# Kernel optimization log

Hardware: AMD Instinct MI355X
Metric: run time of the kernel (lower is better)

The kernel has to match this reference:

```python
import jax, jax.numpy as jnp
import numpy as np
import math

B, L, C = 1, 4096, 1024
H = 16
D = C // H  # head_dim = 64


def setup_inputs() -> dict:
    key = jax.random.key(0)
    ks = jax.random.split(key, 5)
    s = 1.0 / math.sqrt(C)
    return {
        "x": jax.random.normal(ks[0], (B, L, C), dtype=jnp.float32),
        "Wq": jax.random.normal(ks[1], (C, C), dtype=jnp.float32) * s,
        "Wk": jax.random.normal(ks[2], (C, C), dtype=jnp.float32) * s,
        "Wv": jax.random.normal(ks[3], (C, C), dtype=jnp.float32) * s,
        "Wo": jax.random.normal(ks[4], (C, C), dtype=jnp.float32) * s,
    }


def reference(x, Wq, Wk, Wv, Wo):
    # Projections (bias=False). Wq etc. are applied as x @ W (equivalent
    # parameterization to torch Linear's x @ W.T with transposed storage).
    q = (x @ Wq).reshape(B, L, H, D).transpose(0, 2, 1, 3)  # (B,H,L,D)
    k = (x @ Wk).reshape(B, L, H, D).transpose(0, 2, 1, 3)
    v = (x @ Wv).reshape(B, L, H, D).transpose(0, 2, 1, 3)

    scale = 1.0 / math.sqrt(D)
    scores = jnp.einsum("bhqd,bhkd->bhqk", q, k) * scale  # (B,H,L,L)
    causal = jnp.tril(jnp.ones((L, L), dtype=bool))
    scores = jnp.where(causal[None, None, :, :], scores, -jnp.inf)
    probs = jax.nn.softmax(scores, axis=-1)  # dropout p=0 -> identity

    out = jnp.einsum("bhqk,bhkd->bhqd", probs, v)  # (B,H,L,D)
    out = out.transpose(0, 2, 1, 3).reshape(B, L, C)
    return out @ Wo  # resid dropout p=0 -> identity
```

## Files before the change

### kernel.cpp

```cpp
#include <hip/hip_runtime.h>

#define L_SEQ 4096
#define C_DIM 1024
#define H_NUM 16
#define D_HEAD 64
#define LDQK 2048

typedef __bf16 bf16x8 __attribute__((ext_vector_type(8)));
typedef __bf16 bf16x4 __attribute__((ext_vector_type(4)));
typedef float f32x4 __attribute__((ext_vector_type(4)));
typedef float f32x16 __attribute__((ext_vector_type(16)));
typedef unsigned int u32;
typedef u32 u32x4 __attribute__((ext_vector_type(4)));

#define AS1 __attribute__((address_space(1)))
#define AS3 __attribute__((address_space(3)))

#define SC_LOG2E 0.1803368801111204f

__device__ inline __bf16 f2bf(float f) {
  unsigned u = __builtin_bit_cast(unsigned, f);
  u = (u + 0x7fffu + ((u >> 16) & 1u)) >> 16;
  unsigned short s = (unsigned short)u;
  return __builtin_bit_cast(__bf16, s);
}

__device__ inline void gload_lds16(const __bf16* g, __bf16* l) {
  __builtin_amdgcn_global_load_lds((const AS1 void*)g, (AS3 void*)l, 16, 0, 0);
}

__global__ __launch_bounds__(256) void prep(const float* __restrict__ x,
                                            const float* __restrict__ W0,
                                            const float* __restrict__ W1,
                                            const float* __restrict__ W2,
                                            const float* __restrict__ W3,
                                            __bf16* __restrict__ xb,
                                            __bf16* __restrict__ Wt) {
  __shared__ float t[32][33];
  int id = blockIdx.x;
  if (id < 4096) {
    int i = (id * 256 + threadIdx.x) * 4;
    float4 v = *(const float4*)(x + i);
    bf16x4 o = {f2bf(v.x), f2bf(v.y), f2bf(v.z), f2bf(v.w)};
    *(bf16x4*)(xb + i) = o;
    return;
  }
  id -= 4096;
  const int z = id >> 10;
  const int rem = id & 1023;
  const float* W = (z == 0) ? W0 : (z == 1) ? W1 : (z == 2) ? W2 : W3;
  __bf16* dst = Wt + (size_t)z * 1048576;
  const int tx = threadIdx.x & 31, ty = threadIdx.x >> 5;
  const int c0 = (rem & 31) * 32, r0 = (rem >> 5) * 32;
#pragma unroll
  for (int k = 0; k < 4; ++k)
    t[ty + k * 8][tx] = W[(size_t)(r0 + ty + k * 8) * C_DIM + c0 + tx];
  __syncthreads();
#pragma unroll
  for (int k = 0; k < 4; ++k)
    dst[(size_t)(c0 + ty + k * 8) * C_DIM + r0 + tx] = f2bf(t[tx][ty + k * 8]);
}

__global__ __launch_bounds__(256) void gemm_qkv(const __bf16* __restrict__ xb,
                                                const __bf16* __restrict__ WqkT,
                                                const __bf16* __restrict__ WvT,
                                                __bf16* __restrict__ QKb,
                                                __bf16* __restrict__ Vtb) {
  __shared__ __bf16 As[128 * 32];
  __shared__ __bf16 Bs[128 * 32];
  int g = blockIdx.x;
  const __bf16 *A, *Bt;
  __bf16* C;
  int N;
  size_t arow0, brow0;
  float esc;
  if (g < 512) {
    A = xb; Bt = WqkT; C = QKb; N = 2048;
    arow0 = (size_t)(g & 31) * 128;
    brow0 = (size_t)(g >> 5) * 128;
    esc = ((int)brow0 < 1024) ? SC_LOG2E : 1.0f;
  } else {
    g -= 512;
    A = WvT; Bt = xb; C = Vtb; N = 4096;
    arow0 = (size_t)(g & 7) * 128;
    brow0 = (size_t)(g >> 3) * 128;
    esc = 1.0f;
  }
  const int K = 1024;

  const int tid = threadIdx.x;
  const int lane = tid & 63;
  const int wave = tid >> 6;
  const int wm = wave >> 1, wn = wave & 1;
  const int c16 = lane & 15, g4 = lane >> 4;
  const int srow = lane >> 2, scol = (lane & 3) * 8;

  f32x4 acc[4][4] = {};

  for (int kt = 0; kt < K; kt += 32) {
#pragma unroll
    for (int i = 0; i < 2; ++i) {
      const int row = i * 64 + wave * 16 + srow;
      gload_lds16(A + (arow0 + row) * K + kt + scol, As + (i * 64 + wave * 16) * 32);
      gload_lds16(Bt + (brow0 + row) * K + kt + scol, Bs + (i * 64 + wave * 16) * 32);
    }
    __syncthreads();
    bf16x8 af[4], bfr[4];
#pragma unroll
    for (int mi = 0; mi < 4; ++mi)
      af[mi] = *(const bf16x8*)(As + (wm * 64 + mi * 16 + c16) * 32 + g4 * 8);
#pragma unroll
    for (int ni = 0; ni < 4; ++ni)
      bfr[ni] = *(const bf16x8*)(Bs + (wn * 64 + ni * 16 + c16) * 32 + g4 * 8);
#pragma unroll
    for (int mi = 0; mi < 4; ++mi)
#pragma unroll
      for (int ni = 0; ni < 4; ++ni)
        acc[mi][ni] = __builtin_amdgcn_mfma_f32_16x16x32_bf16(af[mi], bfr[ni], acc[mi][ni], 0, 0, 0);
    __syncthreads();
  }

#pragma unroll
  for (int mi = 0; mi < 4; ++mi)
#pragma unroll
    for (int ni = 0; ni < 4; ++ni)
#pragma unroll
      for (int i = 0; i < 4; ++i) {
        size_t row = arow0 + wm * 64 + mi * 16 + g4 * 4 + i;
        size_t col = brow0 + wn * 64 + ni * 16 + c16;
        C[row * N + col] = f2bf(acc[mi][ni][i] * esc);
      }
}

template <bool OUT_BF16>
__global__ __launch_bounds__(256) void gemm_bt(const __bf16* __restrict__ A,
                                               const __bf16* __restrict__ Bt,
                                               void* __restrict__ Cp,
                                               int M, int N, int K,
                                               float cscale, int scale_ncols) {
  __shared__ __bf16 As[128 * 32];
  __shared__ __bf16 Bs[128 * 32];
  const int tid = threadIdx.x;
  const int lane = tid & 63;
  const int wave = tid >> 6;
  const int wm = wave >> 1, wn = wave & 1;
  const int c16 = lane & 15, g4 = lane >> 4;
  const int srow = lane >> 2, scol = (lane & 3) * 8;

  f32x4 acc[4][4] = {};

  const size_t arow0 = (size_t)blockIdx.x * 128;
  const size_t brow0 = (size_t)blockIdx.y * 128;

  for (int kt = 0; kt < K; kt += 32) {
#pragma unroll
    for (int i = 0; i < 2; ++i) {
      const int row = i * 64 + wave * 16 + srow;
      gload_lds16(A + (arow0 + row) * K + kt + scol, As + (i * 64 + wave * 16) * 32);
      gload_lds16(Bt + (brow0 + row) * K + kt + scol, Bs + (i * 64 + wave * 16) * 32);
    }
    __syncthreads();
    bf16x8 af[4], bfr[4];
#pragma unroll
    for (int mi = 0; mi < 4; ++mi)
      af[mi] = *(const bf16x8*)(As + (wm * 64 + mi * 16 + c16) * 32 + g4 * 8);
#pragma unroll
    for (int ni = 0; ni < 4; ++ni)
      bfr[ni] = *(const bf16x8*)(Bs + (wn * 64 + ni * 16 + c16) * 32 + g4 * 8);
#pragma unroll
    for (int mi = 0; mi < 4; ++mi)
#pragma unroll
      for (int ni = 0; ni < 4; ++ni)
        acc[mi][ni] = __builtin_amdgcn_mfma_f32_16x16x32_bf16(af[mi], bfr[ni], acc[mi][ni], 0, 0, 0);
    __syncthreads();
  }

  const float esc = ((int)brow0 < scale_ncols) ? cscale : 1.0f;
#pragma unroll
  for (int mi = 0; mi < 4; ++mi)
#pragma unroll
    for (int ni = 0; ni < 4; ++ni)
#pragma unroll
      for (int i = 0; i < 4; ++i) {
        size_t row = arow0 + wm * 64 + mi * 16 + g4 * 4 + i;
        size_t col = brow0 + wn * 64 + ni * 16 + c16;
        if (OUT_BF16)
          ((__bf16*)Cp)[row * N + col] = f2bf(acc[mi][ni][i] * esc);
        else
          ((float*)Cp)[row * N + col] = acc[mi][ni][i];
      }
}

__global__ __launch_bounds__(256, 1) void attn_fwd(const __bf16* __restrict__ Q,
                                                   const __bf16* __restrict__ Kg,
                                                   const __bf16* __restrict__ Vt,
                                                   __bf16* __restrict__ O) {
  const int bid = blockIdx.x;
  const int h = bid & 15;
  const int p = bid >> 4;
  const int qtA = 31 - p, qtB = p;
  const int ntA = 2 * qtA + 2;
  const int NT = 66;

  __shared__ __bf16 Ks[3][64 * 64];
  __shared__ __bf16 Vs[3][64 * 64];
  __shared__ __bf16 PoS[4][2048];

  const int tid = threadIdx.x;
  const int lane = tid & 63;
  const int wave = tid >> 6;
  const int l31 = lane & 31;
  const int hl = lane >> 5;
  const int rl = lane >> 3;
  const int cs = (lane & 7) ^ rl;

  auto stage = [&](int idx, int b) {
    const int kv = (idx < ntA) ? idx : idx - ntA;
#pragma unroll
    for (int i = 0; i < 2; ++i) {
      const int r = (i * 4 + wave) * 8 + rl;
      gload_lds16(Kg + (size_t)(kv * 64 + r) * LDQK + h * D_HEAD + cs * 8,
                  &Ks[b][(i * 4 + wave) * 512]);
      gload_lds16(Vt + (size_t)(h * D_HEAD + r) * L_SEQ + kv * 64 + cs * 8,
                  &Vs[b][(i * 4 + wave) * 512]);
    }
  };

  int qbase = qtA * 128 + wave * 32;
  bf16x8 qf[4], qfB[4];
  {
    const __bf16* qp = Q + (size_t)(qbase + l31) * LDQK + h * D_HEAD + hl * 8;
#pragma unroll
    for (int s = 0; s < 4; ++s) qf[s] = *(const bf16x8*)(qp + s * 16);
    const __bf16* qp2 = Q + (size_t)(qtB * 128 + wave * 32 + l31) * LDQK + h * D_HEAD + hl * 8;
#pragma unroll
    for (int s = 0; s < 4; ++s) qfB[s] = *(const bf16x8*)(qp2 + s * 16);
  }

  stage(0, 0);
  stage(1, 1);

  int kvmax_w = 2 * qtA + (wave >> 1);
  int q = qbase + l31;

  f32x16 acc0 = {}, acc1 = {};
  float m = -1e30f, lsum = 0.f;
  int bc = 0;

  auto epilogue = [&]() {
    const float rinv = 1.0f / lsum;
    char* const Po = (char*)&PoS[wave][0];
#pragma unroll
    for (int dt = 0; dt < 2; ++dt) {
#pragma unroll
      for (int i = 0; i < 8; ++i) {
        const int r = 2 * i;
        const int d = dt * 32 + (r & 3) + 8 * (r >> 2) + 4 * hl;
        float lo = (dt ? acc1[r] : acc0[r]) * rinv;
        float hi = (dt ? acc1[r + 1] : acc0[r + 1]) * rinv;
        u32 wv;
        asm("v_cvt_pk_bf16_f32 %0, %1, %2" : "=v"(wv) : "v"(lo), "v"(hi));
        *(u32*)(Po + l31 * 128 + (((d >> 3) ^ (l31 & 7)) << 4) + (d & 7) * 2) = wv;
      }
    }
    asm volatile("s_waitcnt lgkmcnt(0)" ::: "memory");
    __builtin_amdgcn_sched_barrier(0);
#pragma unroll
    for (int j = 0; j < 4; ++j) {
      const int qr = lane >> 1;
      const int c = (lane & 1) * 4 + j;
      bf16x8 ov = *(const bf16x8*)(Po + qr * 128 + ((c ^ (qr & 7)) << 4));
      *(bf16x8*)(O + (size_t)(qbase + qr) * C_DIM + h * D_HEAD + c * 8) = ov;
    }
  };

  for (int idx = 0; idx < NT; ++idx) {
    __builtin_amdgcn_sched_barrier(0);
    __builtin_amdgcn_s_barrier();
    __builtin_amdgcn_sched_barrier(0);

    if (idx + 2 < NT) {
      int bs = bc + 2; if (bs >= 3) bs -= 3;
      stage(idx + 2, bs);
      asm volatile("s_waitcnt vmcnt(8)" ::: "memory");
    } else if (idx + 2 == NT) {
      asm volatile("s_waitcnt vmcnt(4)" ::: "memory");
    } else {
      asm volatile("s_waitcnt vmcnt(0)" ::: "memory");
    }
    __builtin_amdgcn_sched_barrier(0);

    const int kvl = (idx < ntA) ? idx : idx - ntA;

    if (kvl <= kvmax_w) {
      char* const KsB = (char*)&Ks[bc][0];
      char* const VsB = (char*)&Vs[bc][0];

      f32x16 st0 = {}, st1 = {};
      __builtin_amdgcn_s_setprio(1);
#pragma unroll
      for (int s = 0; s < 4; ++s) {
        const int ch = s * 2 + hl;
        bf16x8 a0 = *(const bf16x8*)(KsB + l31 * 128 + ((ch ^ (l31 & 7)) << 4));
        bf16x8 a1 = *(const bf16x8*)(KsB + (32 + l31) * 128 + ((ch ^ (l31 & 7)) << 4));
        st0 = __builtin_amdgcn_mfma_f32_32x32x16_bf16(a0, qf[s], st0, 0, 0, 0);
        st1 = __builtin_amdgcn_mfma_f32_32x32x16_bf16(a1, qf[s], st1, 0, 0, 0);
      }
      __builtin_amdgcn_s_setprio(0);

      if (kvl == kvmax_w) {
#pragma unroll
        for (int r = 0; r < 16; ++r) {
          const int kr = (r & 3) + 8 * (r >> 2) + 4 * hl;
          const int k0 = kvl * 64 + kr;
          st0[r] = (k0 <= q) ? st0[r] : -1e30f;
          st1[r] = (k0 + 32 <= q) ? st1[r] : -1e30f;
        }
      }

      float t[16];
#pragma unroll
      for (int r = 0; r < 16; ++r) t[r] = fmaxf(st0[r], st1[r]);
#pragma unroll
      for (int w = 8; w > 0; w >>= 1)
#pragma unroll
        for (int r = 0; r < w; ++r) t[r] = fmaxf(t[r], t[r + w]);
      float mx = fmaxf(t[0], __shfl_xor(t[0], 32, 64));
      const float mnew = fmaxf(m, mx);
      const float corr = exp2f(m - mnew);
      m = mnew;

#pragma unroll
      for (int r = 0; r < 16; ++r) {
        st0[r] = exp2f(st0[r] - m);
        st1[r] = exp2f(st1[r] - m);
      }
      float sm[16];
#pragma unroll
      for (int r = 0; r < 16; ++r) sm[r] = st0[r] + st1[r];
#pragma unroll
      for (int w = 8; w > 0; w >>= 1)
#pragma unroll
        for (int r = 0; r < w; ++r) sm[r] = sm[r] + sm[r + w];
      float sl = sm[0] + __shfl_xor(sm[0], 32, 64);
      lsum = lsum * corr + sl;
      acc0 *= corr;
      acc1 *= corr;

      u32 w0[8], w1[8];
#pragma unroll
      for (int i = 0; i < 8; ++i) {
        asm("v_cvt_pk_bf16_f32 %0, %1, %2" : "=v"(w0[i]) : "v"(st0[2 * i]), "v"(st0[2 * i + 1]));
        asm("v_cvt_pk_bf16_f32 %0, %1, %2" : "=v"(w1[i]) : "v"(st1[2 * i]), "v"(st1[2 * i + 1]));
      }
      u32 e0a = (u32)__shfl_xor((int)(hl ? w0[0] : w0[2]), 32, 64);
      u32 e0b = (u32)__shfl_xor((int)(hl ? w0[1] : w0[3]), 32, 64);
      u32 e0c = (u32)__shfl_xor((int)(hl ? w0[4] : w0[6]), 32, 64);
      u32 e0d = (u32)__shfl_xor((int)(hl ? w0[5] : w0[7]), 32, 64);
      u32 e1a = (u32)__shfl_xor((int)(hl ? w1[0] : w1[2]), 32, 64);
      u32 e1b = (u32)__shfl_xor((int)(hl ? w1[1] : w1[3]), 32, 64);
      u32 e1c = (u32)__shfl_xor((int)(hl ? w1[4] : w1[6]), 32, 64);
      u32 e1d = (u32)__shfl_xor((int)(hl ? w1[5] : w1[7]), 32, 64);
      u32x4 f0 = hl ? (u32x4){e0a, e0b, w0[2], w0[3]} : (u32x4){w0[0], w0[1], e0a, e0b};
      u32x4 f1 = hl ? (u32x4){e0c, e0d, w0[6], w0[7]} : (u32x4){w0[4], w0[5], e0c, e0d};
      u32x4 f2 = hl ? (u32x4){e1a, e1b, w1[2], w1[3]} : (u32x4){w1[0], w1[1], e1a, e1b};
      u32x4 f3 = hl ? (u32x4){e1c, e1d, w1[6], w1[7]} : (u32x4){w1[4], w1[5], e1c, e1d};
      bf16x8 pb0 = __builtin_bit_cast(bf16x8, f0);
      bf16x8 pb1 = __builtin_bit_cast(bf16x8, f1);
      bf16x8 pb2 = __builtin_bit_cast(bf16x8, f2);
      bf16x8 pb3 = __builtin_bit_cast(bf16x8, f3);

      __builtin_amdgcn_s_setprio(1);
#pragma unroll
      for (int s = 0; s < 4; ++s) {
        const bf16x8 pb = (s == 0) ? pb0 : (s == 1) ? pb1 : (s == 2) ? pb2 : pb3;
        const int ch = s * 2 + hl;
        bf16x8 va0 = *(const bf16x8*)(VsB + l31 * 128 + ((ch ^ (l31 & 7)) << 4));
        bf16x8 va1 = *(const bf16x8*)(VsB + (32 + l31) * 128 + ((ch ^ (l31 & 7)) << 4));
        acc0 = __builtin_amdgcn_mfma_f32_32x32x16_bf16(va0, pb, acc0, 0, 0, 0);
        acc1 = __builtin_amdgcn_mfma_f32_32x32x16_bf16(va1, pb, acc1, 0, 0, 0);
      }
      __builtin_amdgcn_s_setprio(0);
    }

    if (idx == ntA - 1) {
      epilogue();
      qbase = qtB * 128 + wave * 32;
      q = qbase + l31;
      kvmax_w = 2 * qtB + (wave >> 1);
#pragma unroll
      for (int s = 0; s < 4; ++s) qf[s] = qfB[s];
      acc0 = (f32x16){};
      acc1 = (f32x16){};
      m = -1e30f;
      lsum = 0.f;
    }

    bc = (bc + 1 == 3) ? 0 : bc + 1;
  }

  epilogue();
}

extern "C" void kernel_launch(void* const* d_in, const int* in_sizes, int n_in,
                              void* d_out, int out_size, void* d_ws, size_t ws_size,
                              hipStream_t stream) {
  const float* x = (const float*)d_in[0];
  const float* Wq = (const float*)d_in[1];
  const float* Wk = (const float*)d_in[2];
  const float* Wv = (const float*)d_in[3];
  const float* Wo = (const float*)d_in[4];
  float* out = (float*)d_out;

  char* ws = (char*)d_ws;
  __bf16* xb    = (__bf16*)(ws);
  __bf16* WqkvT = (__bf16*)(ws + (8u << 20));
  __bf16* QKb   = (__bf16*)(ws + (16u << 20));
  __bf16* Vtb   = (__bf16*)(ws + (32u << 20));
  __bf16* WvT   = WqkvT + (size_t)2 * 1048576;
  __bf16* WoT   = WqkvT + (size_t)3 * 1048576;
  __bf16* Ab    = xb;

  prep<<<8192, 256, 0, stream>>>(x, Wq, Wk, Wv, Wo, xb, WqkvT);

  gemm_qkv<<<768, 256, 0, stream>>>(xb, WqkvT, WvT, QKb, Vtb);

  attn_fwd<<<256, 256, 0, stream>>>(QKb, QKb + 1024, Vtb, Ab);

  gemm_bt<false><<<dim3(32, 8), 256, 0, stream>>>(
      Ab, WoT, out, L_SEQ, C_DIM, C_DIM, 1.0f, 0);
}
```

Before: 275.3 us.

## Split paired-tile attention blocks into one q-tile per block with 2 blocks/CU

Each attention block used to process two complementary query tiles (long and short) in sequence so that work per block stayed balanced. Now each block handles a single 128-row query tile, the grid doubles to 512 blocks, and launch bounds allow 2 blocks per CU so the hardware can overlap them. The K/V prefetch depth also drops from two tiles ahead to one. Block ordering puts the long tiles first, leaving the short tiles to fill in at the end. The risks are tighter register pressure under the 2-blocks-per-CU bound and less latency hiding from the shallower prefetch.

Measured after the change: 241.2 us. -12.4%, faster.

```diff
diff --git a/kernel.cpp b/kernel.cpp
--- a/kernel.cpp
+++ b/kernel.cpp
@@ -191,16 +191,15 @@
       }
 }
 
-__global__ __launch_bounds__(256, 1) void attn_fwd(const __bf16* __restrict__ Q,
+__global__ __launch_bounds__(256, 2) void attn_fwd(const __bf16* __restrict__ Q,
                                                    const __bf16* __restrict__ Kg,
                                                    const __bf16* __restrict__ Vt,
                                                    __bf16* __restrict__ O) {
   const int bid = blockIdx.x;
   const int h = bid & 15;
-  const int p = bid >> 4;
-  const int qtA = 31 - p, qtB = p;
-  const int ntA = 2 * qtA + 2;
-  const int NT = 66;
+  const int g = (bid >> 4) & 15;
+  const int qt = (bid < 256) ? (31 - g) : g;
+  const int nt = 2 * qt + 2;
 
   __shared__ __bf16 Ks[3][64 * 64];
   __shared__ __bf16 Vs[3][64 * 64];
@@ -211,11 +210,14 @@
   const int wave = tid >> 6;
   const int l31 = lane & 31;
   const int hl = lane >> 5;
+  const int qbase = qt * 128 + wave * 32;
+  const int q = qbase + l31;
+  const int kvmax_w = (qbase + 31) >> 6;
+
   const int rl = lane >> 3;
   const int cs = (lane & 7) ^ rl;
 
-  auto stage = [&](int idx, int b) {
-    const int kv = (idx < ntA) ? idx : idx - ntA;
+  auto stage = [&](int kv, int b) {
 #pragma unroll
     for (int i = 0; i < 2; ++i) {
       const int r = (i * 4 + wave) * 8 + rl;
@@ -226,73 +228,32 @@
     }
   };
 
-  int qbase = qtA * 128 + wave * 32;
-  bf16x8 qf[4], qfB[4];
+  bf16x8 qf[4];
   {
-    const __bf16* qp = Q + (size_t)(qbase + l31) * LDQK + h * D_HEAD + hl * 8;
+    const __bf16* qp = Q + (size_t)q * LDQK + h * D_HEAD + hl * 8;
 #pragma unroll
     for (int s = 0; s < 4; ++s) qf[s] = *(const bf16x8*)(qp + s * 16);
-    const __bf16* qp2 = Q + (size_t)(qtB * 128 + wave * 32 + l31) * LDQK + h * D_HEAD + hl * 8;
-#pragma unroll
-    for (int s = 0; s < 4; ++s) qfB[s] = *(const bf16x8*)(qp2 + s * 16);
   }
 
   stage(0, 0);
-  stage(1, 1);
-
-  int kvmax_w = 2 * qtA + (wave >> 1);
-  int q = qbase + l31;
 
   f32x16 acc0 = {}, acc1 = {};
   float m = -1e30f, lsum = 0.f;
+
   int bc = 0;
-
-  auto epilogue = [&]() {
-    const float rinv = 1.0f / lsum;
-    char* const Po = (char*)&PoS[wave][0];
-#pragma unroll
-    for (int dt = 0; dt < 2; ++dt) {
-#pragma unroll
-      for (int i = 0; i < 8; ++i) {
-        const int r = 2 * i;
-        const int d = dt * 32 + (r & 3) + 8 * (r >> 2) + 4 * hl;
-        float lo = (dt ? acc1[r] : acc0[r]) * rinv;
-        float hi = (dt ? acc1[r + 1] : acc0[r + 1]) * rinv;
-        u32 wv;
-        asm("v_cvt_pk_bf16_f32 %0, %1, %2" : "=v"(wv) : "v"(lo), "v"(hi));
-        *(u32*)(Po + l31 * 128 + (((d >> 3) ^ (l31 & 7)) << 4) + (d & 7) * 2) = wv;
-      }
-    }
-    asm volatile("s_waitcnt lgkmcnt(0)" ::: "memory");
-    __builtin_amdgcn_sched_barrier(0);
-#pragma unroll
-    for (int j = 0; j < 4; ++j) {
-      const int qr = lane >> 1;
-      const int c = (lane & 1) * 4 + j;
-      bf16x8 ov = *(const bf16x8*)(Po + qr * 128 + ((c ^ (qr & 7)) << 4));
-      *(bf16x8*)(O + (size_t)(qbase + qr) * C_DIM + h * D_HEAD + c * 8) = ov;
-    }
-  };
-
-  for (int idx = 0; idx < NT; ++idx) {
+  for (int kv = 0; kv < nt; ++kv) {
+    if (kv + 1 < nt) {
+      int bs = bc + 1; if (bs == 3) bs = 0;
+      stage(kv + 1, bs);
+      asm volatile("s_waitcnt vmcnt(4)" ::: "memory");
+    } else {
+      asm volatile("s_waitcnt vmcnt(0)" ::: "memory");
+    }
     __builtin_amdgcn_sched_barrier(0);
     __builtin_amdgcn_s_barrier();
     __builtin_amdgcn_sched_barrier(0);
 
-    if (idx + 2 < NT) {
-      int bs = bc + 2; if (bs >= 3) bs -= 3;
-      stage(idx + 2, bs);
-      asm volatile("s_waitcnt vmcnt(8)" ::: "memory");
-    } else if (idx + 2 == NT) {
-      asm volatile("s_waitcnt vmcnt(4)" ::: "memory");
-    } else {
-      asm volatile("s_waitcnt vmcnt(0)" ::: "memory");
-    }
-    __builtin_amdgcn_sched_barrier(0);
-
-    const int kvl = (idx < ntA) ? idx : idx - ntA;
-
-    if (kvl <= kvmax_w) {
+    if (kv <= kvmax_w) {
       char* const KsB = (char*)&Ks[bc][0];
       char* const VsB = (char*)&Vs[bc][0];
 
@@ -308,11 +269,11 @@
       }
       __builtin_amdgcn_s_setprio(0);
 
-      if (kvl == kvmax_w) {
+      if (kv == kvmax_w) {
 #pragma unroll
         for (int r = 0; r < 16; ++r) {
           const int kr = (r & 3) + 8 * (r >> 2) + 4 * hl;
-          const int k0 = kvl * 64 + kr;
+          const int k0 = kv * 64 + kr;
           st0[r] = (k0 <= q) ? st0[r] : -1e30f;
           st1[r] = (k0 + 32 <= q) ? st1[r] : -1e30f;
         }
@@ -383,23 +344,33 @@
       __builtin_amdgcn_s_setprio(0);
     }
 
-    if (idx == ntA - 1) {
-      epilogue();
-      qbase = qtB * 128 + wave * 32;
-      q = qbase + l31;
-      kvmax_w = 2 * qtB + (wave >> 1);
-#pragma unroll
-      for (int s = 0; s < 4; ++s) qf[s] = qfB[s];
-      acc0 = (f32x16){};
-      acc1 = (f32x16){};
-      m = -1e30f;
-      lsum = 0.f;
-    }
-
-    bc = (bc + 1 == 3) ? 0 : bc + 1;
-  }
-
-  epilogue();
+    bc = bc + 1; if (bc == 3) bc = 0;
+  }
+
+  const float rinv = 1.0f / lsum;
+  char* const Po = (char*)&PoS[wave][0];
+#pragma unroll
+  for (int dt = 0; dt < 2; ++dt) {
+#pragma unroll
+    for (int i = 0; i < 8; ++i) {
+      const int r = 2 * i;
+      const int d = dt * 32 + (r & 3) + 8 * (r >> 2) + 4 * hl;
+      float lo = (dt ? acc1[r] : acc0[r]) * rinv;
+      float hi = (dt ? acc1[r + 1] : acc0[r + 1]) * rinv;
+      u32 wv;
+      asm("v_cvt_pk_bf16_f32 %0, %1, %2" : "=v"(wv) : "v"(lo), "v"(hi));
+      *(u32*)(Po + l31 * 128 + (((d >> 3) ^ (l31 & 7)) << 4) + (d & 7) * 2) = wv;
+    }
+  }
+  asm volatile("s_waitcnt lgkmcnt(0)" ::: "memory");
+  __builtin_amdgcn_sched_barrier(0);
+#pragma unroll
+  for (int j = 0; j < 4; ++j) {
+    const int qr = lane >> 1;
+    const int c = (lane & 1) * 4 + j;
+    bf16x8 ov = *(const bf16x8*)(Po + qr * 128 + ((c ^ (qr & 7)) << 4));
+    *(bf16x8*)(O + (size_t)(qbase + qr) * C_DIM + h * D_HEAD + c * 8) = ov;
+  }
 }
 
 extern "C" void kernel_launch(void* const* d_in, const int* in_sizes, int n_in,
@@ -425,7 +396,7 @@
 
   gemm_qkv<<<768, 256, 0, stream>>>(xb, WqkvT, WvT, QKb, Vtb);
 
-  attn_fwd<<<256, 256, 0, stream>>>(QKb, QKb + 1024, Vtb, Ab);
+  attn_fwd<<<512, 256, 0, stream>>>(QKb, QKb + 1024, Vtb, Ab);
 
   gemm_bt<false><<<dim3(32, 8), 256, 0, stream>>>(
       Ab, WoT, out, L_SEQ, C_DIM, C_DIM, 1.0f, 0);
```
